# Kernel tuning notes

Hardware: AMD Instinct MI355X
Metric: run time of the kernel (lower is better)

## Reference

```python
import jax, jax.numpy as jnp
import numpy as np


def _sparsify24(w):
    """2:4 structured sparsity: per contiguous group of 4 along the last dim,
    keep the 2 largest-magnitude entries, zero the other 2 (soft_threshold24)."""
    m, n = w.shape
    g = w.reshape(m, n // 4, 4)
    a = jnp.abs(g)
    # 2nd-largest magnitude in each group = index 2 of ascending sort of 4
    thresh = jnp.sort(a, axis=-1)[..., 2:3]
    mask = a >= thresh
    return (g * mask).reshape(m, n)


def setup_inputs() -> dict:
    key = jax.random.key(0)
    k1, k2, k3 = jax.random.split(key, 3)
    B, S, DIN, DOUT = 4, 4096, 1024, 1024
    x = jax.random.normal(k1, (B, S, DIN), dtype=jnp.float32)
    weight = jax.random.normal(k2, (DIN, DOUT), dtype=jnp.float32) * 0.02
    bias = jax.random.normal(k3, (DOUT,), dtype=jnp.float32) * 0.02
    sparse_scale = jnp.ones((1,), dtype=jnp.float32)
    return {"x": x, "weight": weight, "bias": bias, "sparse_scale": sparse_scale}


def reference(x, weight, bias, sparse_scale):
    # get_sparse_weight: cast weight to fp16, apply 2:4 sparsity, multiply by
    # learnable fp32 scale (promotes to fp32 as in torch half*float).
    w_sparse = _sparsify24(weight.astype(jnp.float16)).astype(jnp.float32) * sparse_scale
    # fake_fp8_mm: both operands cast to fp16, accumulate/output in fp32.
    a = x.reshape(-1, x.shape[-1]).astype(jnp.float16)          # [B*S, DIN]
    b = w_sparse.astype(jnp.float16)                             # [DIN, DOUT]
    out = jnp.matmul(a, b, preferred_element_type=jnp.float32)   # [B*S, DOUT] fp32
    out = out.reshape(*x.shape[:-1], -1) + bias
    return out
```

## Files before the change

kernel.cpp:

```cpp
#include <hip/hip_runtime.h>
#include <hip/hip_fp16.h>
#include <stdint.h>

#define M_TOT 16384
#define N_TOT 1024
#define K_TOT 1024

typedef _Float16 f16x8 __attribute__((ext_vector_type(8)));
typedef float f32x4 __attribute__((ext_vector_type(4)));
typedef unsigned short ushort4v __attribute__((ext_vector_type(4)));

__device__ inline void gl2lds16(const void* g, void* l) {
    __builtin_amdgcn_global_load_lds(
        (const __attribute__((address_space(1))) void*)(uintptr_t)(g),
        (__attribute__((address_space(3))) void*)(uint32_t)(uintptr_t)(l),
        16, 0, 0);
}

__global__ void __launch_bounds__(256) prep_and_cast(const float* __restrict__ X,
                                                     const float* __restrict__ W,
                                                     const float* __restrict__ scale_p,
                                                     _Float16* __restrict__ Xh,
                                                     _Float16* __restrict__ wT) {
    const int tid = threadIdx.x;
    if (blockIdx.x < 256) {
        __shared__ _Float16 sT[64 * 68 + 4];
        const float scale = scale_p[0];
        const int k0 = (blockIdx.x & 15) * 64;
        const int n0 = (blockIdx.x >> 4) * 64;
        const int r = tid >> 4;
        const int c4 = (tid & 15) * 4;
#pragma unroll
        for (int p = 0; p < 4; ++p) {
            const int k = p * 16 + r;
            float4 w4 = *(const float4*)&W[(size_t)(k0 + k) * N_TOT + n0 + c4];
            _Float16 h0 = (_Float16)w4.x, h1 = (_Float16)w4.y, h2 = (_Float16)w4.z, h3 = (_Float16)w4.w;
            float a0 = fabsf((float)h0), a1 = fabsf((float)h1), a2 = fabsf((float)h2), a3 = fabsf((float)h3);
            float lo01 = fminf(a0, a1), hi01 = fmaxf(a0, a1);
            float lo23 = fminf(a2, a3), hi23 = fmaxf(a2, a3);
            float s2 = fmaxf(fminf(hi01, hi23), fmaxf(lo01, lo23));
            sT[(c4 + 0) * 68 + k] = (_Float16)(((a0 >= s2) ? (float)h0 : 0.0f) * scale);
            sT[(c4 + 1) * 68 + k] = (_Float16)(((a1 >= s2) ? (float)h1 : 0.0f) * scale);
            sT[(c4 + 2) * 68 + k] = (_Float16)(((a2 >= s2) ? (float)h2 : 0.0f) * scale);
            sT[(c4 + 3) * 68 + k] = (_Float16)(((a3 >= s2) ? (float)h3 : 0.0f) * scale);
        }
        __syncthreads();
#pragma unroll
        for (int p = 0; p < 4; ++p) {
            const int n = p * 16 + r;
            ushort4v v = *(const ushort4v*)&sT[n * 68 + c4];
            *(ushort4v*)&wT[(size_t)(n0 + n) * K_TOT + k0 + c4] = v;
        }
    } else {
        size_t i = ((size_t)(blockIdx.x - 256) * 256 + tid) * 8;
        float4 x0 = *(const float4*)&X[i];
        float4 x1 = *(const float4*)&X[i + 4];
        f16x8 h;
        h[0] = (_Float16)x0.x; h[1] = (_Float16)x0.y; h[2] = (_Float16)x0.z; h[3] = (_Float16)x0.w;
        h[4] = (_Float16)x1.x; h[5] = (_Float16)x1.y; h[6] = (_Float16)x1.z; h[7] = (_Float16)x1.w;
        *(f16x8*)&Xh[i] = h;
    }
}

__global__ void __launch_bounds__(512) gemm_bt(const _Float16* __restrict__ A,
                                               const _Float16* __restrict__ Bt,
                                               const float* __restrict__ bias,
                                               float* __restrict__ C) {
    __shared__ _Float16 sA[2][256 * 32];
    __shared__ _Float16 sB[2][128 * 32];
    const int tid = threadIdx.x;
    const int id = blockIdx.x;
    const int by = id & 63;
    const int bx = id >> 6;
    const int wave = tid >> 6;
    const int lane = tid & 63;
    const int wm = wave >> 1;
    const int wn = wave & 1;
    const int quad = lane >> 4;
    const int l16 = lane & 15;

    const int srow = tid >> 2;
    const int scol = (tid & 3) * 8;

    const _Float16* gA = A + ((size_t)(by * 256 + srow)) * K_TOT + scol;
    const _Float16* gB = Bt + ((size_t)(bx * 128 + srow)) * K_TOT + scol;
    const int soff = srow * 32 + scol;

    f32x4 acc[4][4];
#pragma unroll
    for (int i = 0; i < 4; ++i)
#pragma unroll
        for (int j = 0; j < 4; ++j)
            acc[i][j] = (f32x4){0.f, 0.f, 0.f, 0.f};

    for (int k0 = 0; k0 < K_TOT; k0 += 64) {
        __syncthreads();
        gl2lds16(gA + k0,                            &sA[0][soff]);
        gl2lds16(gA + k0 + (size_t)128 * K_TOT,      &sA[0][soff + 128 * 32]);
        gl2lds16(gA + k0 + 32,                       &sA[1][soff]);
        gl2lds16(gA + k0 + 32 + (size_t)128 * K_TOT, &sA[1][soff + 128 * 32]);
        gl2lds16(gB + k0,                            &sB[0][soff]);
        gl2lds16(gB + k0 + 32,                       &sB[1][soff]);
        __syncthreads();

#pragma unroll
        for (int s = 0; s < 2; ++s) {
            f16x8 af[4], bf[4];
#pragma unroll
            for (int i = 0; i < 4; ++i) {
                af[i] = *(const f16x8*)&sA[s][(wm * 64 + i * 16 + l16) * 32 + quad * 8];
                bf[i] = *(const f16x8*)&sB[s][(wn * 64 + i * 16 + l16) * 32 + quad * 8];
            }
#pragma unroll
            for (int i = 0; i < 4; ++i)
#pragma unroll
                for (int j = 0; j < 4; ++j)
                    acc[i][j] = __builtin_amdgcn_mfma_f32_16x16x32_f16(af[i], bf[j], acc[i][j], 0, 0, 0);
        }
    }

#pragma unroll
    for (int j = 0; j < 4; ++j) {
        const int col = bx * 128 + wn * 64 + j * 16 + l16;
        const float bj = bias[col];
#pragma unroll
        for (int i = 0; i < 4; ++i) {
            const int row0 = by * 256 + wm * 64 + i * 16 + quad * 4;
#pragma unroll
            for (int r = 0; r < 4; ++r) {
                C[(size_t)(row0 + r) * N_TOT + col] = acc[i][j][r] + bj;
            }
        }
    }
}

extern "C" void kernel_launch(void* const* d_in, const int* in_sizes, int n_in,
                              void* d_out, int out_size, void* d_ws, size_t ws_size,
                              hipStream_t stream) {
    const float* x      = (const float*)d_in[0];
    const float* weight = (const float*)d_in[1];
    const float* bias   = (const float*)d_in[2];
    const float* sscale = (const float*)d_in[3];
    float* out = (float*)d_out;

    _Float16* wT = (_Float16*)d_ws;
    _Float16* xh = (_Float16*)((char*)d_ws + (size_t)2 * 1024 * 1024);

    prep_and_cast<<<256 + (M_TOT * K_TOT / 8) / 256, 256, 0, stream>>>(x, weight, sscale, xh, wT);
    gemm_bt<<<512, 512, 0, stream>>>(xh, wT, bias, out);
}
```

Before: 149.1 us.

## Use 256x256 GEMM tiles with double-buffered async LDS pipeline and swizzle

Replaces the single-buffered 256x128 GEMM tile loop with a 256x256 tile and a double-buffered LDS pipeline. Global-to-LDS loads for upcoming K slices are issued between MFMA phases, using vmcnt waits and raw barriers. LDS rows are XOR-swizzled to avoid bank conflicts, and s_setprio is raised around MFMA bursts. This halves the grid to 256 blocks and doubles the accumulators per wave, which raises register pressure and leaves fewer blocks than there are CUs.

```diff
diff --git a/kernel.cpp b/kernel.cpp
--- a/kernel.cpp
+++ b/kernel.cpp
@@ -62,76 +62,123 @@
     }
 }
 
-__global__ void __launch_bounds__(512) gemm_bt(const _Float16* __restrict__ A,
-                                               const _Float16* __restrict__ Bt,
-                                               const float* __restrict__ bias,
-                                               float* __restrict__ C) {
-    __shared__ _Float16 sA[2][256 * 32];
-    __shared__ _Float16 sB[2][128 * 32];
+__global__ void __launch_bounds__(512, 2) gemm_bt(const _Float16* __restrict__ A,
+                                                  const _Float16* __restrict__ Bt,
+                                                  const float* __restrict__ bias,
+                                                  float* __restrict__ C) {
+    __shared__ __align__(16) _Float16 sA[2][2][256 * 32];
+    __shared__ __align__(16) _Float16 sB[2][2][256 * 32];
+
     const int tid = threadIdx.x;
     const int id = blockIdx.x;
     const int by = id & 63;
     const int bx = id >> 6;
     const int wave = tid >> 6;
     const int lane = tid & 63;
-    const int wm = wave >> 1;
-    const int wn = wave & 1;
+    const int wm = wave >> 2;
+    const int wn = wave & 3;
     const int quad = lane >> 4;
     const int l16 = lane & 15;
 
-    const int srow = tid >> 2;
-    const int scol = (tid & 3) * 8;
+    const int row0 = tid >> 2;
+    const int s4 = tid & 3;
+    const int g = s4 ^ ((row0 >> 1) & 3);
+    const _Float16* gA = A + (size_t)(by * 256 + row0) * K_TOT + g * 8;
+    const _Float16* gB = Bt + (size_t)(bx * 256 + row0) * K_TOT + g * 8;
+    const int dst0 = row0 * 32 + s4 * 8;
 
-    const _Float16* gA = A + ((size_t)(by * 256 + srow)) * K_TOT + scol;
-    const _Float16* gB = Bt + ((size_t)(bx * 128 + srow)) * K_TOT + scol;
-    const int soff = srow * 32 + scol;
+    const int rdoff = l16 * 64 + ((quad ^ ((l16 >> 1) & 3)) << 4);
 
-    f32x4 acc[4][4];
+    f32x4 acc[8][4];
 #pragma unroll
-    for (int i = 0; i < 4; ++i)
+    for (int i = 0; i < 8; ++i)
 #pragma unroll
         for (int j = 0; j < 4; ++j)
             acc[i][j] = (f32x4){0.f, 0.f, 0.f, 0.f};
+    f16x8 fa[4], fb[4];
 
-    for (int k0 = 0; k0 < K_TOT; k0 += 64) {
-        __syncthreads();
-        gl2lds16(gA + k0,                            &sA[0][soff]);
-        gl2lds16(gA + k0 + (size_t)128 * K_TOT,      &sA[0][soff + 128 * 32]);
-        gl2lds16(gA + k0 + 32,                       &sA[1][soff]);
-        gl2lds16(gA + k0 + 32 + (size_t)128 * K_TOT, &sA[1][soff + 128 * 32]);
-        gl2lds16(gB + k0,                            &sB[0][soff]);
-        gl2lds16(gB + k0 + 32,                       &sB[1][soff]);
-        __syncthreads();
+#define STAGE_A(b, kt, kh) do {                                            \
+        const _Float16* s_ = gA + (kt) * 64 + (kh) * 32;                   \
+        gl2lds16(s_, &sA[b][kh][dst0]);                                    \
+        gl2lds16(s_ + (size_t)128 * K_TOT, &sA[b][kh][dst0 + 128 * 32]);   \
+    } while (0)
+#define STAGE_B(b, kt, kh) do {                                            \
+        const _Float16* s_ = gB + (kt) * 64 + (kh) * 32;                   \
+        gl2lds16(s_, &sB[b][kh][dst0]);                                    \
+        gl2lds16(s_ + (size_t)128 * K_TOT, &sB[b][kh][dst0 + 128 * 32]);   \
+    } while (0)
+#define FENCE asm volatile("" ::: "memory")
+#define WAIT8 asm volatile("s_waitcnt vmcnt(8)" ::: "memory")
+#define BAR do { FENCE; __builtin_amdgcn_s_barrier(); FENCE; } while (0)
 
-#pragma unroll
-        for (int s = 0; s < 2; ++s) {
-            f16x8 af[4], bf[4];
-#pragma unroll
-            for (int i = 0; i < 4; ++i) {
-                af[i] = *(const f16x8*)&sA[s][(wm * 64 + i * 16 + l16) * 32 + quad * 8];
-                bf[i] = *(const f16x8*)&sB[s][(wn * 64 + i * 16 + l16) * 32 + quad * 8];
-            }
-#pragma unroll
-            for (int i = 0; i < 4; ++i)
-#pragma unroll
-                for (int j = 0; j < 4; ++j)
-                    acc[i][j] = __builtin_amdgcn_mfma_f32_16x16x32_f16(af[i], bf[j], acc[i][j], 0, 0, 0);
-        }
+#define PHASE(b, ks, qm, LOADB, STAGE_STMT) do {                                   \
+        {                                                                          \
+            const char* bA_ = (const char*)&sA[b][ks][0] + rdoff + wm * 8192 + (qm) * 4096; \
+            fa[0] = *(const f16x8*)(bA_);                                          \
+            fa[1] = *(const f16x8*)(bA_ + 1024);                                   \
+            fa[2] = *(const f16x8*)(bA_ + 2048);                                   \
+            fa[3] = *(const f16x8*)(bA_ + 3072);                                   \
+            if (LOADB) {                                                           \
+                const char* bB_ = (const char*)&sB[b][ks][0] + rdoff + wn * 4096;  \
+                fb[0] = *(const f16x8*)(bB_);                                      \
+                fb[1] = *(const f16x8*)(bB_ + 1024);                               \
+                fb[2] = *(const f16x8*)(bB_ + 2048);                               \
+                fb[3] = *(const f16x8*)(bB_ + 3072);                               \
+            }                                                                      \
+        }                                                                          \
+        STAGE_STMT;                                                                \
+        BAR;                                                                       \
+        __builtin_amdgcn_s_setprio(1);                                             \
+        _Pragma("unroll")                                                          \
+        for (int ii = 0; ii < 4; ++ii) {                                           \
+            _Pragma("unroll")                                                      \
+            for (int j = 0; j < 4; ++j)                                            \
+                acc[(qm) * 4 + ii][j] = __builtin_amdgcn_mfma_f32_16x16x32_f16(    \
+                    fa[ii], fb[j], acc[(qm) * 4 + ii][j], 0, 0, 0);                \
+        }                                                                          \
+        __builtin_amdgcn_s_setprio(0);                                             \
+    } while (0)
+
+    STAGE_A(0, 0, 0); STAGE_B(0, 0, 0);
+    STAGE_A(0, 0, 1); STAGE_B(0, 0, 1);
+    STAGE_A(1, 1, 0); STAGE_B(1, 1, 0);
+    WAIT8;
+    BAR;
+
+    for (int it = 0; it < 8; ++it) {
+        const int t1 = (2 * it + 1) & 15;
+        const int t2 = (2 * it + 2) & 15;
+        const int t3 = (2 * it + 3) & 15;
+        PHASE(0, 0, 0, 1, STAGE_A(1, t1, 1));        BAR;
+        PHASE(0, 0, 1, 0, STAGE_B(1, t1, 1)); WAIT8; BAR;
+        PHASE(0, 1, 0, 1, STAGE_A(0, t2, 0));        BAR;
+        PHASE(0, 1, 1, 0, STAGE_B(0, t2, 0)); WAIT8; BAR;
+        PHASE(1, 0, 0, 1, STAGE_A(0, t2, 1));        BAR;
+        PHASE(1, 0, 1, 0, STAGE_B(0, t2, 1)); WAIT8; BAR;
+        PHASE(1, 1, 0, 1, STAGE_A(1, t3, 0));        BAR;
+        PHASE(1, 1, 1, 0, STAGE_B(1, t3, 0)); WAIT8; BAR;
     }
 
 #pragma unroll
     for (int j = 0; j < 4; ++j) {
-        const int col = bx * 128 + wn * 64 + j * 16 + l16;
+        const int col = bx * 256 + wn * 64 + j * 16 + l16;
         const float bj = bias[col];
 #pragma unroll
-        for (int i = 0; i < 4; ++i) {
-            const int row0 = by * 256 + wm * 64 + i * 16 + quad * 4;
+        for (int mi = 0; mi < 8; ++mi) {
+            const int row0o = by * 256 + wm * 128 + mi * 16 + quad * 4;
 #pragma unroll
             for (int r = 0; r < 4; ++r) {
-                C[(size_t)(row0 + r) * N_TOT + col] = acc[i][j][r] + bj;
+                C[(size_t)(row0o + r) * N_TOT + col] = acc[mi][j][r] + bj;
             }
         }
     }
+
+#undef PHASE
+#undef BAR
+#undef WAIT8
+#undef FENCE
+#undef STAGE_B
+#undef STAGE_A
 }
 
 extern "C" void kernel_launch(void* const* d_in, const int* in_sizes, int n_in,
@@ -147,5 +194,5 @@
     _Float16* xh = (_Float16*)((char*)d_ws + (size_t)2 * 1024 * 1024);
 
     prep_and_cast<<<256 + (M_TOT * K_TOT / 8) / 256, 256, 0, stream>>>(x, weight, sscale, xh, wT);
-    gemm_bt<<<512, 512, 0, stream>>>(xh, wT, bias, out);
+    gemm_bt<<<256, 512, 0, stream>>>(xh, wT, bias, out);
 }
```

Measured after the change: 152.6 us. 2.4% more time.
